# Kernel optimization log

Measured on AMD Instinct MI355X. Metric: run time of the kernel, lower is better.

## Reference

```python
import jax, jax.numpy as jnp
import numpy as np
import math

D_MODEL = 1024
NUM_HEAD = 16


def setup_inputs() -> dict:
    key = jax.random.key(0)
    k1, k2, k3, k4, k5 = jax.random.split(key, 5)
    B, S, D = 4, 2048, D_MODEL
    lim = 1.0 / math.sqrt(D)
    x = jax.random.normal(k1, (B, S, D), dtype=jnp.float32)
    Wqkv = jax.random.uniform(k2, (D, D), jnp.float32, -lim, lim)
    bqkv = jax.random.uniform(k3, (D,), jnp.float32, -lim, lim)
    Wo = jax.random.uniform(k4, (D, D), jnp.float32, -lim, lim)
    bo = jax.random.uniform(k5, (D,), jnp.float32, -lim, lim)
    return {"x": x, "Wqkv": Wqkv, "bqkv": bqkv, "Wo": Wo, "bo": bo}


def reference(x, Wqkv, bqkv, Wo, bo):
    B, S, D = x.shape
    H = NUM_HEAD
    dk = D // H
    # Single shared linear for Q, K, V (qkv_fc applied to x for all three)
    proj = jnp.einsum('bsd,de->bse', x, Wqkv) + bqkv  # [B,S,D]
    # Faithful to source: raw view(B, H, -1, dk) -- reinterprets memory,
    # NOT a head transpose.
    q = proj.reshape(B, H, S, dk)
    k = q
    v = q
    scores = jnp.einsum('bhqd,bhkd->bhqk', q, k) / math.sqrt(dk)  # [B,H,S,S]
    attn = jax.nn.softmax(scores, axis=-1)
    feats = jnp.einsum('bhqk,bhkd->bhqd', attn, v)  # [B,H,S,dk]
    # transpose(1,2) then view(B, -1, H*dk)
    merged = feats.transpose(0, 2, 1, 3).reshape(B, S, H * dk)
    out = jnp.einsum('bsd,de->bse', merged, Wo) + bo
    return out
```

## Files before the change

### kernel.cpp

```cpp
#include <hip/hip_runtime.h>
#include <hip/hip_bf16.h>

typedef __bf16 bf16;
typedef __attribute__((ext_vector_type(8))) __bf16 bf16x8;
typedef __attribute__((ext_vector_type(4))) float f32x4;
typedef __attribute__((ext_vector_type(16))) float f32x16;

#define MFMA_BF16(a, b, c) __builtin_amdgcn_mfma_f32_16x16x32_bf16((a), (b), (c), 0, 0, 0)
#define MFMA32(a, b, c) __builtin_amdgcn_mfma_f32_32x32x16_bf16((a), (b), (c), 0, 0, 0)
#define EXP2F(x) __builtin_amdgcn_exp2f(x)

__device__ __forceinline__ void gload_lds16(const bf16* g, bf16* l) {
  __builtin_amdgcn_global_load_lds(
      (__attribute__((address_space(1))) void*)(g),
      (__attribute__((address_space(3))) void*)(l), 16, 0, 0);
}

__device__ __forceinline__ int cvtpk(float lo, float hi) {
  int r;
  asm("v_cvt_pk_bf16_f32 %0, %1, %2" : "=v"(r) : "v"(lo), "v"(hi));
  return r;
}

__global__ void transcvt2(const float* __restrict__ W0, bf16* __restrict__ T0,
                          const float* __restrict__ W1, bf16* __restrict__ T1) {
  const float* src = blockIdx.z ? W1 : W0;
  bf16* dst = blockIdx.z ? T1 : T0;
  __shared__ float t[32][33];
  const int bx = blockIdx.x * 32, by = blockIdx.y * 32;
  const int tx = threadIdx.x, ty = threadIdx.y;
#pragma unroll
  for (int i = 0; i < 4; ++i)
    t[ty + i * 8][tx] = src[(long)(by + ty + i * 8) * 1024 + bx + tx];
  __syncthreads();
#pragma unroll
  for (int i = 0; i < 4; ++i)
    dst[(long)(bx + ty + i * 8) * 1024 + by + tx] = (bf16)t[tx][ty + i * 8];
}

template <bool A_IS_F32, bool OUT_F32>
__global__ __launch_bounds__(256) void gemm_bt(const void* __restrict__ Av,
                                               const bf16* __restrict__ Bt,
                                               const float* __restrict__ bias,
                                               void* __restrict__ Cv) {
  __shared__ __align__(16) bf16 As[128 * 32];
  __shared__ __align__(16) bf16 Bs[128 * 32];
  const int tid = threadIdx.x;
  const int l = tid & 63, w = tid >> 6;
  const int wr = w >> 1, wc = w & 1;
  const int lo = l & 15, g = l >> 4;
  const int m0 = blockIdx.x * 128;
  const int n0 = blockIdx.y * 128;
  const bf16* Ab = (const bf16*)Av + (long)m0 * 1024;
  const float* Af = (const float*)Av + (long)m0 * 1024;
  const bf16* Bb = Bt + (long)n0 * 1024;
  const int srow = tid >> 2;
  const int schunk = (tid & 3) * 8;
  f32x4 acc[4][4] = {};
  for (int k0 = 0; k0 < 1024; k0 += 32) {
    __syncthreads();
    if constexpr (A_IS_F32) {
#pragma unroll
      for (int h = 0; h < 2; ++h) {
        const float* p = Af + (long)(srow + h * 64) * 1024 + k0 + schunk;
        f32x4 u0 = *(const f32x4*)p;
        f32x4 u1 = *(const f32x4*)(p + 4);
        bf16x8 vv;
#pragma unroll
        for (int e = 0; e < 4; ++e) {
          vv[e] = (bf16)u0[e];
          vv[4 + e] = (bf16)u1[e];
        }
        *(bf16x8*)&As[h * 2048 + tid * 8] = vv;
      }
    } else {
      gload_lds16(Ab + (long)srow * 1024 + k0 + schunk, As + tid * 8);
      gload_lds16(Ab + (long)(srow + 64) * 1024 + k0 + schunk, As + 2048 + tid * 8);
    }
    gload_lds16(Bb + (long)srow * 1024 + k0 + schunk, Bs + tid * 8);
    gload_lds16(Bb + (long)(srow + 64) * 1024 + k0 + schunk, Bs + 2048 + tid * 8);
    __syncthreads();
    bf16x8 af[4], bfr[4];
#pragma unroll
    for (int m = 0; m < 4; ++m)
      af[m] = *(const bf16x8*)&As[(wr * 64 + m * 16 + lo) * 32 + g * 8];
#pragma unroll
    for (int n = 0; n < 4; ++n)
      bfr[n] = *(const bf16x8*)&Bs[(wc * 64 + n * 16 + lo) * 32 + g * 8];
#pragma unroll
    for (int m = 0; m < 4; ++m)
#pragma unroll
      for (int n = 0; n < 4; ++n)
        acc[m][n] = MFMA_BF16(af[m], bfr[n], acc[m][n]);
  }
#pragma unroll
  for (int n = 0; n < 4; ++n) {
    const int col = n0 + wc * 64 + n * 16 + lo;
    const float bv = bias[col];
#pragma unroll
    for (int m = 0; m < 4; ++m) {
      const long row0 = m0 + wr * 64 + m * 16 + g * 4;
#pragma unroll
      for (int j = 0; j < 4; ++j) {
        if constexpr (OUT_F32)
          ((float*)Cv)[(row0 + j) * 1024 + col] = acc[m][n][j] + bv;
        else
          ((bf16*)Cv)[(row0 + j) * 1024 + col] = (bf16)(acc[m][n][j] + bv);
      }
    }
  }
}

__global__ __launch_bounds__(256) void attn(const bf16* __restrict__ proj,
                                            bf16* __restrict__ merged) {
  __shared__ __align__(16) bf16 Vt[2][64][34];
  const int bid = blockIdx.x;
  const int qb = bid & 15;
  const int hh = (bid >> 4) & 15;
  const int b = bid >> 8;
  const bf16* P = proj + (long)b * 2097152 + (long)hh * 131072;
  const int tid = threadIdx.x;
  const int w = tid >> 6, l = tid & 63;
  const int l31 = l & 31;
  const bool hi = (l >= 32);
  const int hf = hi ? 1 : 0;
  const int qrow = qb * 128 + w * 32;

  const int skv = tid >> 3;
  const int sc = (tid & 7) * 8;

  const float QSCALE = 0.125f * 1.44269504088896f;
  bf16x8 qf[4];
#pragma unroll
  for (int s = 0; s < 4; ++s) {
    bf16x8 t = *(const bf16x8*)&P[(long)(qrow + l31) * 64 + s * 16 + hf * 8];
#pragma unroll
    for (int e = 0; e < 8; ++e) t[e] = (bf16)((float)t[e] * QSCALE);
    qf[s] = t;
  }

  f32x16 o0 = {}, o1 = {};
  float mq = -1e30f, lq = 0.f;

  bf16x8 kA[4], kB[4];
  {
    bf16x8 v = *(const bf16x8*)&P[(long)skv * 64 + sc];
#pragma unroll
    for (int e = 0; e < 8; ++e) Vt[0][sc + e][skv] = v[e];
  }
#pragma unroll
  for (int s = 0; s < 4; ++s)
    kA[s] = *(const bf16x8*)&P[(long)l31 * 64 + s * 16 + hf * 8];
  __syncthreads();

  for (int t2 = 0; t2 < 32; ++t2) {
#pragma unroll
    for (int ph = 0; ph < 2; ++ph) {
      const int t = t2 * 2 + ph;
      const int tn = (t < 63) ? t + 1 : 63;
      bf16x8 vnx = *(const bf16x8*)&P[((long)tn * 32 + skv) * 64 + sc];
      f32x16 s;
      if (ph == 0) {
        s = MFMA32(kA[0], qf[0], f32x16{});
        s = MFMA32(kA[1], qf[1], s);
        s = MFMA32(kA[2], qf[2], s);
        s = MFMA32(kA[3], qf[3], s);
      } else {
        s = MFMA32(kB[0], qf[0], f32x16{});
        s = MFMA32(kB[1], qf[1], s);
        s = MFMA32(kB[2], qf[2], s);
        s = MFMA32(kB[3], qf[3], s);
      }
#pragma unroll
      for (int sx = 0; sx < 4; ++sx) {
        bf16x8 kv8 = *(const bf16x8*)&P[((long)tn * 32 + l31) * 64 + sx * 16 + hf * 8];
        if (ph == 0) kB[sx] = kv8; else kA[sx] = kv8;
      }
      float mx = s[0];
#pragma unroll
      for (int i = 1; i < 16; ++i) mx = fmaxf(mx, s[i]);
      mx = fmaxf(mx, __shfl_xor(mx, 32));
      if (__any(mx > mq)) {
        const float mnew = fmaxf(mq, mx);
        const float corr = EXP2F(mq - mnew);
        mq = mnew;
        lq *= corr;
#pragma unroll
        for (int i = 0; i < 16; ++i) { o0[i] *= corr; o1[i] *= corr; }
      }
      float ps = 0.f;
#pragma unroll
      for (int i = 0; i < 16; ++i) {
        const float p = EXP2F(s[i] - mq);
        s[i] = p;
        ps += p;
      }
      ps += __shfl_xor(ps, 32);
      lq += ps;
      const int pk0 = cvtpk(s[0], s[1]), pk1 = cvtpk(s[2], s[3]);
      const int pk2 = cvtpk(s[4], s[5]), pk3 = cvtpk(s[6], s[7]);
      const int pk4 = cvtpk(s[8], s[9]), pk5 = cvtpk(s[10], s[11]);
      const int pk6 = cvtpk(s[12], s[13]), pk7 = cvtpk(s[14], s[15]);
      const int x0 = __shfl_xor(pk0, 32), x2 = __shfl_xor(pk2, 32);
      const int x1 = __shfl_xor(pk1, 32), x3 = __shfl_xor(pk3, 32);
      const int x4 = __shfl_xor(pk4, 32), x6 = __shfl_xor(pk6, 32);
      const int x5 = __shfl_xor(pk5, 32), x7 = __shfl_xor(pk7, 32);
      int bi0[4], bi1[4];
      bi0[0] = hi ? x2 : pk0;
      bi0[1] = hi ? x3 : pk1;
      bi0[2] = hi ? pk2 : x0;
      bi0[3] = hi ? pk3 : x1;
      bi1[0] = hi ? x6 : pk4;
      bi1[1] = hi ? x7 : pk5;
      bi1[2] = hi ? pk6 : x4;
      bi1[3] = hi ? pk7 : x5;
      bf16x8 pb0 = *(bf16x8*)bi0;
      bf16x8 pb1 = *(bf16x8*)bi1;
      {
        bf16x8 va;
        va = *(const bf16x8*)&Vt[ph][l31][hf * 8];
        o0 = MFMA32(va, pb0, o0);
        va = *(const bf16x8*)&Vt[ph][l31][16 + hf * 8];
        o0 = MFMA32(va, pb1, o0);
        va = *(const bf16x8*)&Vt[ph][32 + l31][hf * 8];
        o1 = MFMA32(va, pb0, o1);
        va = *(const bf16x8*)&Vt[ph][32 + l31][16 + hf * 8];
        o1 = MFMA32(va, pb1, o1);
      }
#pragma unroll
      for (int e = 0; e < 8; ++e) Vt[ph ^ 1][sc + e][skv] = vnx[e];
      __syncthreads();
    }
  }

  const float inv = 1.0f / lq;
  bf16* mb = merged + (long)b * 2097152 + hh * 64;
  const long rowoff = (long)(qrow + l31) * 1024;
  const int dbase[8] = {0, 2, 8, 10, 16, 18, 24, 26};
#pragma unroll
  for (int r = 0; r < 8; ++r) {
    const int d = dbase[r] + 4 * hf;
    *(int*)&mb[rowoff + d] = cvtpk(o0[2 * r] * inv, o0[2 * r + 1] * inv);
    *(int*)&mb[rowoff + 32 + d] = cvtpk(o1[2 * r] * inv, o1[2 * r + 1] * inv);
  }
}

extern "C" void kernel_launch(void* const* d_in, const int* in_sizes, int n_in,
                              void* d_out, int out_size, void* d_ws, size_t ws_size,
                              hipStream_t stream) {
  const float* x = (const float*)d_in[0];
  const float* Wqkv = (const float*)d_in[1];
  const float* bqkv = (const float*)d_in[2];
  const float* Wo = (const float*)d_in[3];
  const float* bo = (const float*)d_in[4];
  float* out = (float*)d_out;

  char* ws = (char*)d_ws;
  bf16* proj = (bf16*)(ws);
  bf16* merged = (bf16*)(ws + 16777216);
  bf16* WqkvT = (bf16*)(ws + 33554432);
  bf16* WoT = (bf16*)(ws + 35651584);

  transcvt2<<<dim3(32, 32, 2), dim3(32, 8), 0, stream>>>(Wqkv, WqkvT, Wo, WoT);
  gemm_bt<true, false><<<dim3(64, 8), dim3(256), 0, stream>>>(x, WqkvT, bqkv, proj);
  attn<<<dim3(1024), dim3(256), 0, stream>>>(proj, merged);
  gemm_bt<false, true><<<dim3(64, 8), dim3(256), 0, stream>>>(merged, WoT, bo, out);
}
```

Baseline: 327.0 us.

## Use permlane32 swaps for softmax reductions and repack V transpose with packed LDS writes

Replaces the cross-half __shfl_xor operations (max, sum, and the P-fragment exchange) with v_permlane32_swap instructions. A runtime probe picks the swap direction. The V tile transpose into LDS now loads pairs of kv rows as 4-element chunks and writes packed 32-bit words, replacing the eight 16-bit scatter stores per thread. The goal is to cut ds_bpermute/LDS traffic and bank conflicts in the inner attention loop. The cost is reliance on inline asm semantics and more global load instructions, each of which is narrower.

```diff
diff --git a/kernel.cpp b/kernel.cpp
--- a/kernel.cpp
+++ b/kernel.cpp
@@ -5,6 +5,7 @@
 typedef __attribute__((ext_vector_type(8))) __bf16 bf16x8;
 typedef __attribute__((ext_vector_type(4))) float f32x4;
 typedef __attribute__((ext_vector_type(16))) float f32x16;
+typedef __attribute__((ext_vector_type(4))) unsigned short u16x4;
 
 #define MFMA_BF16(a, b, c) __builtin_amdgcn_mfma_f32_16x16x32_bf16((a), (b), (c), 0, 0, 0)
 #define MFMA32(a, b, c) __builtin_amdgcn_mfma_f32_32x32x16_bf16((a), (b), (c), 0, 0, 0)
@@ -20,6 +21,21 @@
   int r;
   asm("v_cvt_pk_bf16_f32 %0, %1, %2" : "=v"(r) : "v"(lo), "v"(hi));
   return r;
+}
+__device__ __forceinline__ void plswap(int& a, int& b) {
+  asm volatile("v_permlane32_swap_b32 %0, %1" : "+v"(a), "+v"(b));
+}
+__device__ __forceinline__ float swap_max(float x) {
+  int u = __float_as_int(x), v;
+  asm volatile("v_mov_b32 %0, %1" : "=v"(v) : "v"(u));
+  plswap(u, v);
+  return fmaxf(__int_as_float(u), __int_as_float(v));
+}
+__device__ __forceinline__ float swap_add(float x) {
+  int u = __float_as_int(x), v;
+  asm volatile("v_mov_b32 %0, %1" : "=v"(v) : "v"(u));
+  plswap(u, v);
+  return __int_as_float(u) + __int_as_float(v);
 }
 
 __global__ void transcvt2(const float* __restrict__ W0, bf16* __restrict__ T0,
@@ -122,12 +138,17 @@
   const int tid = threadIdx.x;
   const int w = tid >> 6, l = tid & 63;
   const int l31 = l & 31;
-  const bool hi = (l >= 32);
-  const int hf = hi ? 1 : 0;
+  const int hf = l >> 5;
   const int qrow = qb * 128 + w * 32;
 
-  const int skv = tid >> 3;
-  const int sc = (tid & 7) * 8;
+  const int kvp = tid >> 4;
+  const int dc = tid & 15;
+  int* VtI = (int*)Vt;
+
+  int pu = l, pv;
+  asm volatile("v_mov_b32 %0, %1" : "=v"(pv) : "v"(pu));
+  plswap(pu, pv);
+  const bool dir1 = (__shfl(pu, 33, 64) == 1);
 
   const float QSCALE = 0.125f * 1.44269504088896f;
   bf16x8 qf[4];
@@ -144,9 +165,11 @@
 
   bf16x8 kA[4], kB[4];
   {
-    bf16x8 v = *(const bf16x8*)&P[(long)skv * 64 + sc];
-#pragma unroll
-    for (int e = 0; e < 8; ++e) Vt[0][sc + e][skv] = v[e];
+    u16x4 v0 = *(const u16x4*)&P[(long)(2 * kvp) * 64 + dc * 4];
+    u16x4 v1 = *(const u16x4*)&P[(long)(2 * kvp + 1) * 64 + dc * 4];
+#pragma unroll
+    for (int dd = 0; dd < 4; ++dd)
+      VtI[(dc * 4 + dd) * 17 + kvp] = ((int)v0[dd]) | (((int)v1[dd]) << 16);
   }
 #pragma unroll
   for (int s = 0; s < 4; ++s)
@@ -158,7 +181,8 @@
     for (int ph = 0; ph < 2; ++ph) {
       const int t = t2 * 2 + ph;
       const int tn = (t < 63) ? t + 1 : 63;
-      bf16x8 vnx = *(const bf16x8*)&P[((long)tn * 32 + skv) * 64 + sc];
+      u16x4 vn0 = *(const u16x4*)&P[((long)tn * 32 + 2 * kvp) * 64 + dc * 4];
+      u16x4 vn1 = *(const u16x4*)&P[((long)tn * 32 + 2 * kvp + 1) * 64 + dc * 4];
       f32x16 s;
       if (ph == 0) {
         s = MFMA32(kA[0], qf[0], f32x16{});
@@ -179,7 +203,7 @@
       float mx = s[0];
 #pragma unroll
       for (int i = 1; i < 16; ++i) mx = fmaxf(mx, s[i]);
-      mx = fmaxf(mx, __shfl_xor(mx, 32));
+      mx = swap_max(mx);
       if (__any(mx > mq)) {
         const float mnew = fmaxf(mq, mx);
         const float corr = EXP2F(mq - mnew);
@@ -195,25 +219,19 @@
         s[i] = p;
         ps += p;
       }
-      ps += __shfl_xor(ps, 32);
+      ps = swap_add(ps);
       lq += ps;
-      const int pk0 = cvtpk(s[0], s[1]), pk1 = cvtpk(s[2], s[3]);
-      const int pk2 = cvtpk(s[4], s[5]), pk3 = cvtpk(s[6], s[7]);
-      const int pk4 = cvtpk(s[8], s[9]), pk5 = cvtpk(s[10], s[11]);
-      const int pk6 = cvtpk(s[12], s[13]), pk7 = cvtpk(s[14], s[15]);
-      const int x0 = __shfl_xor(pk0, 32), x2 = __shfl_xor(pk2, 32);
-      const int x1 = __shfl_xor(pk1, 32), x3 = __shfl_xor(pk3, 32);
-      const int x4 = __shfl_xor(pk4, 32), x6 = __shfl_xor(pk6, 32);
-      const int x5 = __shfl_xor(pk5, 32), x7 = __shfl_xor(pk7, 32);
-      int bi0[4], bi1[4];
-      bi0[0] = hi ? x2 : pk0;
-      bi0[1] = hi ? x3 : pk1;
-      bi0[2] = hi ? pk2 : x0;
-      bi0[3] = hi ? pk3 : x1;
-      bi1[0] = hi ? x6 : pk4;
-      bi1[1] = hi ? x7 : pk5;
-      bi1[2] = hi ? pk6 : x4;
-      bi1[3] = hi ? pk7 : x5;
+      int p0 = cvtpk(s[0], s[1]), p1 = cvtpk(s[2], s[3]);
+      int p2 = cvtpk(s[4], s[5]), p3 = cvtpk(s[6], s[7]);
+      int p4 = cvtpk(s[8], s[9]), p5 = cvtpk(s[10], s[11]);
+      int p6 = cvtpk(s[12], s[13]), p7 = cvtpk(s[14], s[15]);
+      if (dir1) {
+        plswap(p0, p2); plswap(p1, p3); plswap(p4, p6); plswap(p5, p7);
+      } else {
+        plswap(p2, p0); plswap(p3, p1); plswap(p6, p4); plswap(p7, p5);
+      }
+      int bi0[4] = {p0, p1, p2, p3};
+      int bi1[4] = {p4, p5, p6, p7};
       bf16x8 pb0 = *(bf16x8*)bi0;
       bf16x8 pb1 = *(bf16x8*)bi1;
       {
@@ -227,8 +245,12 @@
         va = *(const bf16x8*)&Vt[ph][32 + l31][16 + hf * 8];
         o1 = MFMA32(va, pb1, o1);
       }
-#pragma unroll
-      for (int e = 0; e < 8; ++e) Vt[ph ^ 1][sc + e][skv] = vnx[e];
+      {
+        int* W = VtI + (ph ^ 1) * (64 * 17);
+#pragma unroll
+        for (int dd = 0; dd < 4; ++dd)
+          W[(dc * 4 + dd) * 17 + kvp] = ((int)vn0[dd]) | (((int)vn1[dd]) << 16);
+      }
       __syncthreads();
     }
   }
```

Result: no change. 326.8 us (-0.1%).
